# Performance work log

Measured on AMD Instinct MI355X. Metric: run time of the kernel, lower is better.

Reference implementation:

```python
import jax, jax.numpy as jnp
import numpy as np

B = 8        # number of clouds
NP = 4096    # points per cloud
STRIDE = 4   # sampler stride -> NS = NP // STRIDE sampled centers per cloud
K = 32       # knn neighbours
NS = NP // STRIDE


def setup_inputs() -> dict:
    key = jax.random.key(0)
    k1, k2, k3, k4 = jax.random.split(key, 4)
    N = B * NP
    x = jax.random.normal(k1, (N, 64), dtype=jnp.float32)
    pos = jax.random.normal(k2, (N, 3), dtype=jnp.float32)
    batch = jnp.repeat(jnp.arange(B, dtype=jnp.int64), NP)
    d_in = 64 + 3
    W1 = jax.random.normal(k3, (d_in, 128), dtype=jnp.float32) / np.sqrt(d_in)
    b1 = jnp.zeros((128,), dtype=jnp.float32)
    W2 = jax.random.normal(k4, (128, 256), dtype=jnp.float32) / np.sqrt(128)
    b2 = jnp.zeros((256,), dtype=jnp.float32)
    return {"x": x, "pos": pos, "batch": batch, "W1": W1, "b1": b1, "W2": W2, "b2": b2}


def reference(x, pos, batch, W1, b1, W2, b2):
    # --- sampler: stride sampling per cloud (clouds are equal-sized, contiguous) ---
    pos_b = pos.reshape(B, NP, 3)
    idx_local = jnp.arange(0, NP, STRIDE)                       # [NS]
    idx = (idx_local[None, :] + jnp.arange(B)[:, None] * NP).reshape(-1)  # global sampled idx [B*NS]
    pos_s = pos_b[:, idx_local]                                 # [B, NS, 3]

    # --- neighbour_finder: knn within each cloud (batch-respecting via per-cloud blocks) ---
    # squared distances [B, NS, NP] without materializing [B,NS,NP,3]
    d2 = ((pos_s ** 2).sum(-1)[:, :, None]
          + (pos_b ** 2).sum(-1)[:, None, :]
          - 2.0 * jnp.einsum('bsd,bnd->bsn', pos_s, pos_b))
    _, nbr = jax.lax.top_k(-d2, K)                              # [B, NS, K] local neighbour idx
    col = (nbr + (jnp.arange(B) * NP)[:, None, None]).reshape(-1)  # global neighbour idx [E]

    # --- conv: PointNetConv -> MLP(concat(x_j, pos_j - pos_i)) then max over neighbours ---
    x_j = x[col].reshape(B, NS, K, -1)                          # [B, NS, K, 64]
    rel = pos[col].reshape(B, NS, K, 3) - pos_s[:, :, None, :]  # pos_j - pos_i
    feat = jnp.concatenate([x_j, rel], axis=-1)                 # [B, NS, K, 67]
    h = jax.nn.relu(feat @ W1 + b1)                             # [B, NS, K, 128]
    h = jax.nn.relu(h @ W2 + b2)                                # [B, NS, K, 256]
    x_out = h.max(axis=2).reshape(B * NS, -1)                   # [B*NS, 256]

    pos_out = pos_s.reshape(-1, 3)
    batch_out = batch[idx]
    return x_out, pos_out, batch_out, idx
```

## Files before the change

### kernel.cpp

```cpp
#include <hip/hip_runtime.h>
#include <hip/hip_bf16.h>

#define BB 8
#define NP 4096
#define STRIDE 4
#define KNN 32
#define NS (NP/STRIDE)
#define NQ (BB*NS)
#define DIN 67
#define H1N 128
#define H2N 256
#define WCAP 512

typedef __attribute__((ext_vector_type(8)))  short bf16x8;
typedef __attribute__((ext_vector_type(16))) float f32x16;
typedef __attribute__((ext_vector_type(8)))  short short8;

__device__ __forceinline__ unsigned int f2u(float f) {
    unsigned int b = __float_as_uint(f);
    return (b & 0x80000000u) ? ~b : (b | 0x80000000u);
}
__device__ __forceinline__ short f2bf(float f) {
    unsigned u = __float_as_uint(f);
    unsigned r = u + 0x7FFFu + ((u >> 16) & 1u);
    return (short)(r >> 16);
}
__device__ __forceinline__ int pack2(float a, float b) {
    return (int)((unsigned short)f2bf(a) | ((unsigned)(unsigned short)f2bf(b) << 16));
}

__global__ __launch_bounds__(256) void fused_kernel(const float* __restrict__ pos,
                                                    const float* __restrict__ x,
                                                    const short* __restrict__ W1T,
                                                    const short* __restrict__ W2T,
                                                    const float* __restrict__ b1,
                                                    const float* __restrict__ b2,
                                                    float* __restrict__ out) {
    __shared__ __align__(16) unsigned long long surv[4 * WCAP];
    __shared__ unsigned int pvt[4];
    __shared__ int cnts[4];
    __shared__ int col_l[KNN];

    const int q    = blockIdx.x;
    const int b    = q >> 10;
    const int s    = q & (NS - 1);
    const int qi   = b * NP + s * STRIDE;
    const int t    = threadIdx.x;
    const int w    = t >> 6;
    const int lane = t & 63;

    if (t < 5) {
        float* pos_out   = out + (size_t)NQ * H2N;
        float* batch_out = pos_out + (size_t)NQ * 3;
        float* idx_out   = batch_out + NQ;
        if (t < 3)       pos_out[q*3+t] = pos[qi*3+t];
        else if (t == 3) batch_out[q] = (float)b;
        else             idx_out[q]   = (float)qi;
    }

    const float qx = pos[qi*3+0], qy = pos[qi*3+1], qz = pos[qi*3+2];
    const float q2 = __fadd_rn(__fadd_rn(__fmul_rn(qx,qx), __fmul_rn(qy,qy)), __fmul_rn(qz,qz));

    const float* pb = pos + (size_t)b * NP * 3;
    unsigned int myk[16];
    #pragma unroll
    for (int i = 0; i < 4; ++i) {
        const int u = t + i * 256;
        const float4* pp = (const float4*)(pb + (size_t)u * 12);
        const float4 v0 = pp[0], v1 = pp[1], v2 = pp[2];
        const float px[4] = {v0.x, v0.w, v1.z, v2.y};
        const float py[4] = {v0.y, v1.x, v1.w, v2.z};
        const float pz[4] = {v0.z, v1.y, v2.x, v2.w};
        #pragma unroll
        for (int j = 0; j < 4; ++j) {
            const float p2 = __fadd_rn(__fadd_rn(__fmul_rn(px[j],px[j]), __fmul_rn(py[j],py[j])), __fmul_rn(pz[j],pz[j]));
            const float dt = __fadd_rn(__fadd_rn(__fmul_rn(qx,px[j]), __fmul_rn(qy,py[j])), __fmul_rn(qz,pz[j]));
            const float d2 = __fsub_rn(__fadd_rn(q2, p2), __fmul_rn(2.0f, dt));
            myk[i*4+j] = f2u(d2);
        }
    }

    if (t < 64) {
        const unsigned int mk = myk[0];
        int rank = 0;
        #pragma unroll
        for (int ss = 0; ss < 64; ++ss) {
            const unsigned int ks = (unsigned int)__shfl((int)mk, ss, 64);
            rank += (int)((ks < mk) | ((ks == mk) & (ss < t)));
        }
        if (rank == 1)  pvt[0] = mk;
        if (rank == 3)  pvt[1] = mk;
        if (rank == 8)  pvt[2] = mk;
        if (rank == 31) pvt[3] = mk;
    }
    __syncthreads();

    int cw;
    {
        const unsigned int T = pvt[0];
        int base = 0;
        #pragma unroll
        for (int i = 0; i < 16; ++i) {
            const bool p = (myk[i] <= T);
            const unsigned long long mask = __ballot(p);
            if (p) {
                const int off = base + (int)__popcll(mask & ((1ull << lane) - 1ull));
                if (off < WCAP) {
                    const int n = 4 * (t + (i >> 2) * 256) + (i & 3);
                    surv[(w << 9) + off] = ((unsigned long long)myk[i] << 32) | (unsigned int)n;
                }
            }
            base += (int)__popcll(mask);
        }
        cw = (base < WCAP) ? base : WCAP;
    }
    if (lane == 0) cnts[w] = cw;
    __syncthreads();

    int c0 = cnts[0], c1 = cnts[1], c2 = cnts[2], c3 = cnts[3];
    int C = c0 + c1 + c2 + c3;

    if (C < KNN) {
        int level;
        for (level = 1; level < 4; ++level) {
            const unsigned int T = pvt[level];
            int cnt = 0;
            #pragma unroll
            for (int i = 0; i < 16; ++i)
                cnt += (int)__popcll(__ballot(myk[i] <= T));
            if (lane == 0) cnts[w] = cnt;
            __syncthreads();
            C = cnts[0] + cnts[1] + cnts[2] + cnts[3];
            if (C >= KNN) break;
            __syncthreads();
        }
        if (level > 3) level = 3;
        __syncthreads();
        {
            const unsigned int T = pvt[level];
            int base = 0;
            #pragma unroll
            for (int i = 0; i < 16; ++i) {
                const bool p = (myk[i] <= T);
                const unsigned long long mask = __ballot(p);
                if (p) {
                    const int off = base + (int)__popcll(mask & ((1ull << lane) - 1ull));
                    if (off < WCAP) {
                        const int n = 4 * (t + (i >> 2) * 256) + (i & 3);
                        surv[(w << 9) + off] = ((unsigned long long)myk[i] << 32) | (unsigned int)n;
                    }
                }
                base += (int)__popcll(mask);
            }
            cw = (base < WCAP) ? base : WCAP;
        }
        if (lane == 0) cnts[w] = cw;
        __syncthreads();
        c0 = cnts[0]; c1 = cnts[1]; c2 = cnts[2]; c3 = cnts[3];
        C = c0 + c1 + c2 + c3;
    }

    {
        const int cwp = (cw + 7) & ~7;
        for (int i = cw + lane; i < cwp; i += 64)
            surv[(w << 9) + i] = ~0ull;
    }
    __syncthreads();

    const int s1 = c0, s2 = c0 + c1, s3 = c0 + c1 + c2;
    const int cseg[4] = {c0, c1, c2, c3};
    for (int j = t; j < C; j += 256) {
        const int seg = (int)(j >= s1) + (int)(j >= s2) + (int)(j >= s3);
        const int off = j - ((seg == 0) ? 0 : (seg == 1) ? s1 : (seg == 2) ? s2 : s3);
        const unsigned long long v = surv[(seg << 9) + off];
        int rk = 0;
        #pragma unroll 1
        for (int k = 0; k < 4; ++k) {
            const int np = ((cseg[k] + 7) & ~7) >> 1;
            const ulonglong2* sp = (const ulonglong2*)(surv + (k << 9));
            #pragma unroll 4
            for (int ss = 0; ss < np; ++ss) {
                const ulonglong2 pr = sp[ss];
                rk += (int)(pr.x < v) + (int)(pr.y < v);
            }
        }
        if (rk < KNN)
            col_l[rk] = b * NP + (int)(unsigned int)(v & 0xFFFFFFFFull);
    }
    __syncthreads();

    short* feat = (short*)surv;
    short* h1s  = ((short*)surv) + 2560;

    {
        const int row = t >> 3, part = t & 7;
        const int c   = col_l[row];
        const float4* xr = (const float4*)(x + (size_t)c * 64 + part * 8);
        const float4 v0 = xr[0], v1 = xr[1];
        short* fr = feat + row * 80 + part * 8;
        *(int*)(fr + 0) = pack2(v0.x, v0.y);
        *(int*)(fr + 2) = pack2(v0.z, v0.w);
        *(int*)(fr + 4) = pack2(v1.x, v1.y);
        *(int*)(fr + 6) = pack2(v1.z, v1.w);
        if (part == 0) {
            short8 o;
            o[0] = f2bf(pos[c*3+0] - qx);
            o[1] = f2bf(pos[c*3+1] - qy);
            o[2] = f2bf(pos[c*3+2] - qz);
            o[3] = 0; o[4] = 0; o[5] = 0; o[6] = 0; o[7] = 0;
            *(short8*)(feat + row * 80 + 64) = o;
            short8 z = {0,0,0,0,0,0,0,0};
            *(short8*)(feat + row * 80 + 72) = z;
        }
    }
    __syncthreads();

    const int lr2 = lane & 31;
    const int lh  = lane >> 5;

    {
        bf16x8 w1f[5];
        #pragma unroll
        for (int kt = 0; kt < 5; ++kt)
            w1f[kt] = *(const bf16x8*)(W1T + ((size_t)(w*5 + kt) * 64 + lane) * 8);

        bf16x8 a1[5];
        #pragma unroll
        for (int kt = 0; kt < 5; ++kt)
            a1[kt] = *(const bf16x8*)(feat + lr2 * 80 + 16*kt + 8*lh);

        const float bv = b1[32*w + lr2];
        f32x16 acc;
        #pragma unroll
        for (int r = 0; r < 16; ++r) acc[r] = bv;
        #pragma unroll
        for (int kt = 0; kt < 5; ++kt)
            acc = __builtin_amdgcn_mfma_f32_32x32x16_bf16(a1[kt], w1f[kt], acc, 0, 0, 0);

        #pragma unroll
        for (int r = 0; r < 16; ++r) {
            const int i = (r & 3) + 8*(r >> 2) + 4*lh;
            const int c = 32*w + lr2;
            const int adr = i * 128 + ((((c >> 3) ^ (i & 15)) << 3) | (c & 7));
            h1s[adr] = f2bf(fmaxf(acc[r], 0.0f));
        }
    }
    __syncthreads();

    {
        bf16x8 a2[8];
        #pragma unroll
        for (int kt = 0; kt < 8; ++kt) {
            const int slot = 2*kt + lh;
            a2[kt] = *(const bf16x8*)(h1s + lr2 * 128 + ((slot ^ (lr2 & 15)) << 3));
        }

        #pragma unroll
        for (int half = 0; half < 2; ++half) {
            const int nt = w + 4*half;
            bf16x8 wf[8];
            #pragma unroll
            for (int kt = 0; kt < 8; ++kt)
                wf[kt] = *(const bf16x8*)(W2T + ((size_t)(nt*8 + kt) * 64 + lane) * 8);
            f32x16 acc;
            #pragma unroll
            for (int r = 0; r < 16; ++r) acc[r] = 0.0f;
            #pragma unroll
            for (int kt = 0; kt < 8; ++kt)
                acc = __builtin_amdgcn_mfma_f32_32x32x16_bf16(a2[kt], wf[kt], acc, 0, 0, 0);

            float m = acc[0];
            #pragma unroll
            for (int r = 1; r < 16; ++r) m = fmaxf(m, acc[r]);
            m = fmaxf(m, __shfl_xor(m, 32, 64));
            m = fmaxf(m + b2[32*nt + lr2], 0.0f);
            if (lane < 32) out[(size_t)q * H2N + 32*nt + lane] = m;
        }
    }
}

__global__ __launch_bounds__(64) void prep_w(const float* __restrict__ W1,
                                             const float* __restrict__ W2,
                                             short* __restrict__ W1T,
                                             short* __restrict__ W2T) {
    const int l = threadIdx.x;
    if (blockIdx.x < 20) {
        const int nt = blockIdx.x / 5, t = blockIdx.x % 5;
        const int c  = 32*nt + (l & 31);
        short8 v;
        #pragma unroll
        for (int b = 0; b < 8; ++b) {
            const int k = 16*t + 8*(l >> 5) + b;
            v[b] = (k < DIN) ? f2bf(W1[k * H1N + c]) : (short)0;
        }
        *(short8*)(W1T + ((size_t)(nt*5 + t) * 64 + l) * 8) = v;
    } else {
        const int bb = blockIdx.x - 20;
        const int nt = bb >> 3, t = bb & 7;
        const int c  = 32*nt + (l & 31);
        short8 v;
        #pragma unroll
        for (int b = 0; b < 8; ++b) {
            const int k = 16*t + 8*(l >> 5) + b;
            v[b] = f2bf(W2[k * H2N + c]);
        }
        *(short8*)(W2T + ((size_t)(nt*8 + t) * 64 + l) * 8) = v;
    }
}

extern "C" void kernel_launch(void* const* d_in, const int* in_sizes, int n_in,
                              void* d_out, int out_size, void* d_ws, size_t ws_size,
                              hipStream_t stream) {
    const float* x   = (const float*)d_in[0];
    const float* pos = (const float*)d_in[1];
    const float* W1  = (const float*)d_in[3];
    const float* b1  = (const float*)d_in[4];
    const float* W2  = (const float*)d_in[5];
    const float* b2  = (const float*)d_in[6];
    float* out = (float*)d_out;

    char* ws   = (char*)d_ws;
    short* W1T = (short*)ws;
    short* W2T = (short*)(ws + 20480);

    prep_w<<<84, 64, 0, stream>>>(W1, W2, W1T, W2T);
    fused_kernel<<<NQ, 256, 0, stream>>>(pos, x, W1T, W2T, b1, b2, out);
}
```

Measured before the change: 129.1 us.

## Double block size to 512 threads and spread KNN and MLP over eight waves

Each query block now runs 512 threads in eight waves. Each thread scores 8 points instead of 16, and per-wave survivor buffers shrink to 256 entries. The rank selection walks eight segments, the gather uses 16 threads per neighbour row, and each wave computes one 32-column tile of the second layer instead of two. The first layer runs only in waves 0-3. The aim is more parallelism per query and less serial work per thread, at the cost of more block-wide synchronisation and possibly lower occupancy from the larger shared buffer and block.

```diff
diff --git a/kernel.cpp b/kernel.cpp
--- a/kernel.cpp
+++ b/kernel.cpp
@@ -10,7 +10,7 @@
 #define DIN 67
 #define H1N 128
 #define H2N 256
-#define WCAP 512
+#define WCAP 256
 
 typedef __attribute__((ext_vector_type(8)))  short bf16x8;
 typedef __attribute__((ext_vector_type(16))) float f32x16;
@@ -29,16 +29,16 @@
     return (int)((unsigned short)f2bf(a) | ((unsigned)(unsigned short)f2bf(b) << 16));
 }
 
-__global__ __launch_bounds__(256) void fused_kernel(const float* __restrict__ pos,
+__global__ __launch_bounds__(512) void fused_kernel(const float* __restrict__ pos,
                                                     const float* __restrict__ x,
                                                     const short* __restrict__ W1T,
                                                     const short* __restrict__ W2T,
                                                     const float* __restrict__ b1,
                                                     const float* __restrict__ b2,
                                                     float* __restrict__ out) {
-    __shared__ __align__(16) unsigned long long surv[4 * WCAP];
+    __shared__ __align__(16) unsigned long long surv[8 * WCAP];
     __shared__ unsigned int pvt[4];
-    __shared__ int cnts[4];
+    __shared__ int cnts[8];
     __shared__ int col_l[KNN];
 
     const int q    = blockIdx.x;
@@ -62,10 +62,10 @@
     const float q2 = __fadd_rn(__fadd_rn(__fmul_rn(qx,qx), __fmul_rn(qy,qy)), __fmul_rn(qz,qz));
 
     const float* pb = pos + (size_t)b * NP * 3;
-    unsigned int myk[16];
+    unsigned int myk[8];
     #pragma unroll
-    for (int i = 0; i < 4; ++i) {
-        const int u = t + i * 256;
+    for (int i = 0; i < 2; ++i) {
+        const int u = t + i * 512;
         const float4* pp = (const float4*)(pb + (size_t)u * 12);
         const float4 v0 = pp[0], v1 = pp[1], v2 = pp[2];
         const float px[4] = {v0.x, v0.w, v1.z, v2.y};
@@ -100,14 +100,14 @@
         const unsigned int T = pvt[0];
         int base = 0;
         #pragma unroll
-        for (int i = 0; i < 16; ++i) {
+        for (int i = 0; i < 8; ++i) {
             const bool p = (myk[i] <= T);
             const unsigned long long mask = __ballot(p);
             if (p) {
                 const int off = base + (int)__popcll(mask & ((1ull << lane) - 1ull));
                 if (off < WCAP) {
-                    const int n = 4 * (t + (i >> 2) * 256) + (i & 3);
-                    surv[(w << 9) + off] = ((unsigned long long)myk[i] << 32) | (unsigned int)n;
+                    const int n = 4 * (t + (i >> 2) * 512) + (i & 3);
+                    surv[(w << 8) + off] = ((unsigned long long)myk[i] << 32) | (unsigned int)n;
                 }
             }
             base += (int)__popcll(mask);
@@ -117,8 +117,7 @@
     if (lane == 0) cnts[w] = cw;
     __syncthreads();
 
-    int c0 = cnts[0], c1 = cnts[1], c2 = cnts[2], c3 = cnts[3];
-    int C = c0 + c1 + c2 + c3;
+    int C = cnts[0] + cnts[1] + cnts[2] + cnts[3] + cnts[4] + cnts[5] + cnts[6] + cnts[7];
 
     if (C < KNN) {
         int level;
@@ -126,11 +125,11 @@
             const unsigned int T = pvt[level];
             int cnt = 0;
             #pragma unroll
-            for (int i = 0; i < 16; ++i)
+            for (int i = 0; i < 8; ++i)
                 cnt += (int)__popcll(__ballot(myk[i] <= T));
             if (lane == 0) cnts[w] = cnt;
             __syncthreads();
-            C = cnts[0] + cnts[1] + cnts[2] + cnts[3];
+            C = cnts[0] + cnts[1] + cnts[2] + cnts[3] + cnts[4] + cnts[5] + cnts[6] + cnts[7];
             if (C >= KNN) break;
             __syncthreads();
         }
@@ -140,14 +139,14 @@
             const unsigned int T = pvt[level];
             int base = 0;
             #pragma unroll
-            for (int i = 0; i < 16; ++i) {
+            for (int i = 0; i < 8; ++i) {
                 const bool p = (myk[i] <= T);
                 const unsigned long long mask = __ballot(p);
                 if (p) {
                     const int off = base + (int)__popcll(mask & ((1ull << lane) - 1ull));
                     if (off < WCAP) {
-                        const int n = 4 * (t + (i >> 2) * 256) + (i & 3);
-                        surv[(w << 9) + off] = ((unsigned long long)myk[i] << 32) | (unsigned int)n;
+                        const int n = 4 * (t + (i >> 2) * 512) + (i & 3);
+                        surv[(w << 8) + off] = ((unsigned long long)myk[i] << 32) | (unsigned int)n;
                     }
                 }
                 base += (int)__popcll(mask);
@@ -156,36 +155,45 @@
         }
         if (lane == 0) cnts[w] = cw;
         __syncthreads();
-        c0 = cnts[0]; c1 = cnts[1]; c2 = cnts[2]; c3 = cnts[3];
-        C = c0 + c1 + c2 + c3;
+        C = cnts[0] + cnts[1] + cnts[2] + cnts[3] + cnts[4] + cnts[5] + cnts[6] + cnts[7];
     }
 
     {
         const int cwp = (cw + 7) & ~7;
         for (int i = cw + lane; i < cwp; i += 64)
-            surv[(w << 9) + i] = ~0ull;
-    }
-    __syncthreads();
-
-    const int s1 = c0, s2 = c0 + c1, s3 = c0 + c1 + c2;
-    const int cseg[4] = {c0, c1, c2, c3};
-    for (int j = t; j < C; j += 256) {
-        const int seg = (int)(j >= s1) + (int)(j >= s2) + (int)(j >= s3);
-        const int off = j - ((seg == 0) ? 0 : (seg == 1) ? s1 : (seg == 2) ? s2 : s3);
-        const unsigned long long v = surv[(seg << 9) + off];
-        int rk = 0;
-        #pragma unroll 1
-        for (int k = 0; k < 4; ++k) {
-            const int np = ((cseg[k] + 7) & ~7) >> 1;
-            const ulonglong2* sp = (const ulonglong2*)(surv + (k << 9));
-            #pragma unroll 4
-            for (int ss = 0; ss < np; ++ss) {
-                const ulonglong2 pr = sp[ss];
-                rk += (int)(pr.x < v) + (int)(pr.y < v);
+            surv[(w << 8) + i] = ~0ull;
+    }
+    __syncthreads();
+
+    {
+        int cn[8];
+        #pragma unroll
+        for (int k = 0; k < 8; ++k) cn[k] = cnts[k];
+
+        for (int j = t; j < C; j += 512) {
+            int off = j, seg = 0;
+            bool cont = true;
+            #pragma unroll
+            for (int k = 0; k < 7; ++k) {
+                const bool step = cont && (off >= cn[k]);
+                if (step) off -= cn[k]; else cont = false;
+                seg += (int)step;
             }
-        }
-        if (rk < KNN)
-            col_l[rk] = b * NP + (int)(unsigned int)(v & 0xFFFFFFFFull);
+            const unsigned long long v = surv[(seg << 8) + off];
+            int rk = 0;
+            #pragma unroll 1
+            for (int k = 0; k < 8; ++k) {
+                const int np = ((cn[k] + 7) & ~7) >> 1;
+                const ulonglong2* sp = (const ulonglong2*)(surv + (k << 8));
+                #pragma unroll 4
+                for (int ss = 0; ss < np; ++ss) {
+                    const ulonglong2 pr = sp[ss];
+                    rk += (int)(pr.x < v) + (int)(pr.y < v);
+                }
+            }
+            if (rk < KNN)
+                col_l[rk] = b * NP + (int)(unsigned int)(v & 0xFFFFFFFFull);
+        }
     }
     __syncthreads();
 
@@ -193,15 +201,12 @@
     short* h1s  = ((short*)surv) + 2560;
 
     {
-        const int row = t >> 3, part = t & 7;
+        const int row = t >> 4, part = t & 15;
         const int c   = col_l[row];
-        const float4* xr = (const float4*)(x + (size_t)c * 64 + part * 8);
-        const float4 v0 = xr[0], v1 = xr[1];
-        short* fr = feat + row * 80 + part * 8;
-        *(int*)(fr + 0) = pack2(v0.x, v0.y);
-        *(int*)(fr + 2) = pack2(v0.z, v0.w);
-        *(int*)(fr + 4) = pack2(v1.x, v1.y);
-        *(int*)(fr + 6) = pack2(v1.z, v1.w);
+        const float4 v = ((const float4*)(x + (size_t)c * 64))[part];
+        short* fr = feat + row * 80 + part * 4;
+        *(int*)(fr + 0) = pack2(v.x, v.y);
+        *(int*)(fr + 2) = pack2(v.z, v.w);
         if (part == 0) {
             short8 o;
             o[0] = f2bf(pos[c*3+0] - qx);
@@ -218,7 +223,7 @@
     const int lr2 = lane & 31;
     const int lh  = lane >> 5;
 
-    {
+    if (w < 4) {
         bf16x8 w1f[5];
         #pragma unroll
         for (int kt = 0; kt < 5; ++kt)
@@ -255,27 +260,24 @@
             a2[kt] = *(const bf16x8*)(h1s + lr2 * 128 + ((slot ^ (lr2 & 15)) << 3));
         }
 
-        #pragma unroll
-        for (int half = 0; half < 2; ++half) {
-            const int nt = w + 4*half;
-            bf16x8 wf[8];
-            #pragma unroll
-            for (int kt = 0; kt < 8; ++kt)
-                wf[kt] = *(const bf16x8*)(W2T + ((size_t)(nt*8 + kt) * 64 + lane) * 8);
-            f32x16 acc;
-            #pragma unroll
-            for (int r = 0; r < 16; ++r) acc[r] = 0.0f;
-            #pragma unroll
-            for (int kt = 0; kt < 8; ++kt)
-                acc = __builtin_amdgcn_mfma_f32_32x32x16_bf16(a2[kt], wf[kt], acc, 0, 0, 0);
-
-            float m = acc[0];
-            #pragma unroll
-            for (int r = 1; r < 16; ++r) m = fmaxf(m, acc[r]);
-            m = fmaxf(m, __shfl_xor(m, 32, 64));
-            m = fmaxf(m + b2[32*nt + lr2], 0.0f);
-            if (lane < 32) out[(size_t)q * H2N + 32*nt + lane] = m;
-        }
+        bf16x8 wf[8];
+        #pragma unroll
+        for (int kt = 0; kt < 8; ++kt)
+            wf[kt] = *(const bf16x8*)(W2T + ((size_t)(w*8 + kt) * 64 + lane) * 8);
+
+        f32x16 acc;
+        #pragma unroll
+        for (int r = 0; r < 16; ++r) acc[r] = 0.0f;
+        #pragma unroll
+        for (int kt = 0; kt < 8; ++kt)
+            acc = __builtin_amdgcn_mfma_f32_32x32x16_bf16(a2[kt], wf[kt], acc, 0, 0, 0);
+
+        float m = acc[0];
+        #pragma unroll
+        for (int r = 1; r < 16; ++r) m = fmaxf(m, acc[r]);
+        m = fmaxf(m, __shfl_xor(m, 32, 64));
+        m = fmaxf(m + b2[32*w + lr2], 0.0f);
+        if (lane < 32) out[(size_t)q * H2N + 32*w + lane] = m;
     }
 }
 
@@ -324,5 +326,5 @@
     short* W2T = (short*)(ws + 20480);
 
     prep_w<<<84, 64, 0, stream>>>(W1, W2, W1T, W2T);
-    fused_kernel<<<NQ, 256, 0, stream>>>(pos, x, W1T, W2T, b1, b2, out);
-}
+    fused_kernel<<<NQ, 512, 0, stream>>>(pos, x, W1T, W2T, b1, b2, out);
+}
```

Measured after the change: 173.2 us. 34.2% more time.
